# Performance work log

Hardware: AMD Instinct MI355X
Metric: run time of the kernel (lower is better)

Reference implementation:

```python
import jax, jax.numpy as jnp
import numpy as np

N_EVENTS = 4_000_000
HW = 128          # DVS sensor resolution
TICKS = 10_000    # simulation horizon
KH, KW = 3, 3     # kernel_size
OUT_CH = 64       # out_channels


def setup_inputs() -> dict:
    key = jax.random.key(0)
    k1, k2, k3 = jax.random.split(key, 3)
    return {
        "values": jnp.ones((N_EVENTS,), dtype=jnp.float32),            # spike value 1.0 per add_spike
        "ticks_in": jax.random.randint(k1, (N_EVENTS,), 0, TICKS, dtype=jnp.int32),
        "xs": jax.random.randint(k2, (N_EVENTS,), 0, HW, dtype=jnp.int32),
        "ys": jax.random.randint(k3, (N_EVENTS,), 0, HW, dtype=jnp.int32),
        "stride": 1,
    }


def reference(values, ticks_in, xs, ys, stride):
    """Event-driven spike routing of Conv2dT.forward.

    Returns the per-channel synapse input buffers [OUT_CH, KH*KW, TICKS]:
    buffer[c, s, t] = total spike value scattered into synapse s of soma c at tick t.
    (The subsequent izh-soma ODE simulation lives in the external ABM model.)
    """
    S = KH * KW
    off_y = jnp.repeat(jnp.arange(KH), KW)   # [S], ky per synapse_idx = ky*KW + kx
    off_x = jnp.tile(jnp.arange(KW), KH)     # [S], kx per synapse_idx

    out_x = xs[None, :] - off_x[:, None]     # [S, N]
    out_y = ys[None, :] - off_y[:, None]     # [S, N]
    valid = (out_x >= 0) & (out_y >= 0) & (out_x % stride == 0) & (out_y % stride == 0)
    contrib = jnp.where(valid, values[None, :], jnp.zeros((), values.dtype))  # [S, N]

    # scatter-add over ticks for each synapse offset
    buf = jnp.zeros((S, TICKS), dtype=values.dtype)
    buf = buf.at[jnp.arange(S)[:, None], ticks_in[None, :]].add(contrib)     # [S, T]

    # every output channel receives the identical spike dispatch
    return jnp.broadcast_to(buf[None], (OUT_CH, S, TICKS))
```

## Files before the change

### kernel.cpp

```cpp
#include <hip/hip_runtime.h>

#define TICKS 10000
#define NSYN 9
#define OUT_CH 64

#define NPART 32
#define SCATTER_BLOCKS 512
#define SCATTER_THREADS 1024

__global__ void zero_kernel(float* __restrict__ p, int n) {
    int i = blockIdx.x * blockDim.x + threadIdx.x;
    if (i < n) p[i] = 0.0f;
}

__global__ __launch_bounds__(SCATTER_THREADS) void scatter_kernel(
    const float* __restrict__ values,
    const int*   __restrict__ ticks,
    const int*   __restrict__ xs,
    const int*   __restrict__ ys,
    const int*   __restrict__ stride_p,
    float*       __restrict__ buf,
    float*       __restrict__ part,
    int P,
    int n)
{
    __shared__ float lhist[TICKS];
    const int stride = stride_p[0];
    const int tid = threadIdx.x;

    if (stride == 1) {
        for (int j = tid; j < TICKS; j += SCATTER_THREADS) lhist[j] = 0.0f;
        __syncthreads();

        const int n4  = n >> 2;
        const int gsz = gridDim.x * SCATTER_THREADS;
        const float4* __restrict__ v4 = (const float4*)values;
        const int4*   __restrict__ t4 = (const int4*)ticks;
        const int4*   __restrict__ x4 = (const int4*)xs;
        const int4*   __restrict__ y4 = (const int4*)ys;

        for (int i = blockIdx.x * SCATTER_THREADS + tid; i < n4; i += gsz) {
            float4 v = v4[i];
            int4   t = t4[i];
            int4   x = x4[i];
            int4   y = y4[i];

            if (x.x >= 2 && y.x >= 2) atomicAdd(&lhist[t.x], v.x);
            else atomicAdd(&buf[(min(y.x, 2) * 3 + min(x.x, 2)) * TICKS + t.x], v.x);

            if (x.y >= 2 && y.y >= 2) atomicAdd(&lhist[t.y], v.y);
            else atomicAdd(&buf[(min(y.y, 2) * 3 + min(x.y, 2)) * TICKS + t.y], v.y);

            if (x.z >= 2 && y.z >= 2) atomicAdd(&lhist[t.z], v.z);
            else atomicAdd(&buf[(min(y.z, 2) * 3 + min(x.z, 2)) * TICKS + t.z], v.z);

            if (x.w >= 2 && y.w >= 2) atomicAdd(&lhist[t.w], v.w);
            else atomicAdd(&buf[(min(y.w, 2) * 3 + min(x.w, 2)) * TICKS + t.w], v.w);
        }

        if ((n & 3) && blockIdx.x == 0 && tid == 0) {
            for (int i = n4 << 2; i < n; ++i) {
                int cls = min(ys[i], 2) * 3 + min(xs[i], 2);
                if (cls == 8) atomicAdd(&part[ticks[i]], values[i]);
                else          atomicAdd(&buf[cls * TICKS + ticks[i]], values[i]);
            }
        }

        __syncthreads();

        float* __restrict__ dst = part + (size_t)(blockIdx.x % P) * TICKS;
        int phase = ((blockIdx.x / P) * 613) % TICKS;
        for (int j = tid; j < TICKS; j += SCATTER_THREADS) {
            int b = j + phase;
            if (b >= TICKS) b -= TICKS;
            float v = lhist[b];
            if (v != 0.0f) atomicAdd(&dst[b], v);
        }
    } else {
        const int gsz = gridDim.x * SCATTER_THREADS;
        for (int i = blockIdx.x * SCATTER_THREADS + tid; i < n; i += gsz) {
            float v = values[i];
            int   t = ticks[i];
            int   x = xs[i];
            int   y = ys[i];
            #pragma unroll
            for (int ky = 0; ky < 3; ++ky) {
                int oy = y - ky;
                if (oy < 0 || (oy % stride) != 0) continue;
                #pragma unroll
                for (int kx = 0; kx < 3; ++kx) {
                    int ox = x - kx;
                    if (ox < 0 || (ox % stride) != 0) continue;
                    atomicAdd(&buf[(ky * 3 + kx) * TICKS + t], v);
                }
            }
        }
    }
}

__global__ __launch_bounds__(256) void combine_kernel(
    float*       __restrict__ buf,
    const float* __restrict__ part,
    const int*   __restrict__ stride_p,
    int P)
{
    int t = blockIdx.x * blockDim.x + threadIdx.x;
    if (t >= TICKS) return;
    const int stride = stride_p[0];

    float b[NSYN];
    #pragma unroll
    for (int s = 0; s < NSYN; ++s) b[s] = buf[s * TICKS + t];

    if (stride == 1) {
        float s8 = 0.0f;
        for (int p = 0; p < P; ++p) s8 += part[(size_t)p * TICKS + t];
        b[8] = s8;
        #pragma unroll
        for (int r = 0; r < 3; ++r) {
            b[r * 3 + 1] += b[r * 3 + 2];
            b[r * 3 + 0] += b[r * 3 + 1];
        }
        #pragma unroll
        for (int c = 0; c < 3; ++c) {
            b[3 + c] += b[6 + c];
            b[0 + c] += b[3 + c];
        }
    }

    #pragma unroll
    for (int s = 0; s < NSYN; ++s) buf[s * TICKS + t] = b[s];
}

__global__ __launch_bounds__(256) void emit_kernel(
    const float* __restrict__ buf,
    float*       __restrict__ out)
{
    const int T4 = TICKS / 4;
    int t = blockIdx.x * blockDim.x + threadIdx.x;
    if (t >= T4) return;

    const float4* __restrict__ b4 = (const float4*)buf;
    float4*       __restrict__ o4 = (float4*)out;

    float4 b[NSYN];
    #pragma unroll
    for (int s = 0; s < NSYN; ++s) b[s] = b4[s * T4 + t];

    for (int c = blockIdx.y; c < OUT_CH; c += gridDim.y) {
        #pragma unroll
        for (int s = 0; s < NSYN; ++s) {
            o4[(c * NSYN + s) * T4 + t] = b[s];
        }
    }
}

extern "C" void kernel_launch(void* const* d_in, const int* in_sizes, int n_in,
                              void* d_out, int out_size, void* d_ws, size_t ws_size,
                              hipStream_t stream) {
    const float* values   = (const float*)d_in[0];
    const int*   ticks    = (const int*)  d_in[1];
    const int*   xs       = (const int*)  d_in[2];
    const int*   ys       = (const int*)  d_in[3];
    const int*   stride_p = (const int*)  d_in[4];
    float*       out      = (float*)      d_out;
    const int n = in_sizes[0];

    const size_t need = (size_t)(NSYN + NPART) * TICKS * sizeof(float);
    float* buf;
    float* part;
    int    P;
    bool   fallback;
    if (ws_size >= need) {
        buf = (float*)d_ws;
        part = buf + (size_t)NSYN * TICKS;
        P = NPART;
        fallback = false;
    } else {
        buf = out;
        part = buf + (size_t)8 * TICKS;
        P = 1;
        fallback = true;
    }

    {
        int nz = (fallback ? NSYN : (NSYN + NPART)) * TICKS;
        zero_kernel<<<(nz + 255) / 256, 256, 0, stream>>>(buf, nz);
    }

    scatter_kernel<<<SCATTER_BLOCKS, SCATTER_THREADS, 0, stream>>>(
        values, ticks, xs, ys, stride_p, buf, part, P, n);

    combine_kernel<<<(TICKS + 255) / 256, 256, 0, stream>>>(buf, part, stride_p, P);

    {
        dim3 grid((TICKS / 4 + 255) / 256, fallback ? 1 : 64);
        emit_kernel<<<grid, 256, 0, stream>>>(buf, out);
    }
}
```

Baseline: 146.7 us.

## Write per-block tick histograms directly and reduce them in a split combine pass

Each scatter block now stores its full shared-memory histogram to its own partial row with plain float4 stores, replacing atomic adds into a small set of shared partial rows. The scatter grid is halved so there are fewer rows to reduce. A 2D combine kernel sums slices of rows and atomically adds them into synapse 8. The prefix-sum fold over the 3x3 synapse grid moves into the emit kernel. This removes global atomic contention at the end of the scatter, and in exchange it writes and re-reads 256 full histogram rows (about 10 MB) and adds atomics in the combine.

```diff
diff --git a/kernel.cpp b/kernel.cpp
--- a/kernel.cpp
+++ b/kernel.cpp
@@ -4,9 +4,9 @@
 #define NSYN 9
 #define OUT_CH 64
 
-#define NPART 32
-#define SCATTER_BLOCKS 512
+#define SCATTER_BLOCKS 256
 #define SCATTER_THREADS 1024
+#define COMBINE_BY 8
 
 __global__ void zero_kernel(float* __restrict__ p, int n) {
     int i = blockIdx.x * blockDim.x + threadIdx.x;
@@ -61,20 +61,25 @@
         if ((n & 3) && blockIdx.x == 0 && tid == 0) {
             for (int i = n4 << 2; i < n; ++i) {
                 int cls = min(ys[i], 2) * 3 + min(xs[i], 2);
-                if (cls == 8) atomicAdd(&part[ticks[i]], values[i]);
-                else          atomicAdd(&buf[cls * TICKS + ticks[i]], values[i]);
+                atomicAdd(&buf[cls * TICKS + ticks[i]], values[i]);
             }
         }
 
         __syncthreads();
 
-        float* __restrict__ dst = part + (size_t)(blockIdx.x % P) * TICKS;
-        int phase = ((blockIdx.x / P) * 613) % TICKS;
-        for (int j = tid; j < TICKS; j += SCATTER_THREADS) {
-            int b = j + phase;
-            if (b >= TICKS) b -= TICKS;
-            float v = lhist[b];
-            if (v != 0.0f) atomicAdd(&dst[b], v);
+        if (P > 0) {
+            const float4* __restrict__ l4 = (const float4*)lhist;
+            float4* __restrict__ dst = (float4*)(part + (size_t)blockIdx.x * TICKS);
+            const int T4 = TICKS / 4;
+            for (int j = tid; j < T4; j += SCATTER_THREADS) dst[j] = l4[j];
+        } else {
+            int phase = (blockIdx.x * 157) % TICKS;
+            for (int j = tid; j < TICKS; j += SCATTER_THREADS) {
+                int b = j + phase;
+                if (b >= TICKS) b -= TICKS;
+                float v = lhist[b];
+                if (v != 0.0f) atomicAdd(&buf[8 * TICKS + b], v);
+            }
         }
     } else {
         const int gsz = gridDim.x * SCATTER_THREADS;
@@ -104,41 +109,36 @@
     const int*   __restrict__ stride_p,
     int P)
 {
-    int t = blockIdx.x * blockDim.x + threadIdx.x;
-    if (t >= TICKS) return;
-    const int stride = stride_p[0];
-
-    float b[NSYN];
-    #pragma unroll
-    for (int s = 0; s < NSYN; ++s) b[s] = buf[s * TICKS + t];
-
-    if (stride == 1) {
-        float s8 = 0.0f;
-        for (int p = 0; p < P; ++p) s8 += part[(size_t)p * TICKS + t];
-        b[8] = s8;
-        #pragma unroll
-        for (int r = 0; r < 3; ++r) {
-            b[r * 3 + 1] += b[r * 3 + 2];
-            b[r * 3 + 0] += b[r * 3 + 1];
-        }
-        #pragma unroll
-        for (int c = 0; c < 3; ++c) {
-            b[3 + c] += b[6 + c];
-            b[0 + c] += b[3 + c];
-        }
-    }
-
-    #pragma unroll
-    for (int s = 0; s < NSYN; ++s) buf[s * TICKS + t] = b[s];
+    if (stride_p[0] != 1 || P <= 0) return;
+    const int T4 = TICKS / 4;
+    int t4 = blockIdx.x * blockDim.x + threadIdx.x;
+    if (t4 >= T4) return;
+
+    const int rows = P / COMBINE_BY;
+    const int r0   = blockIdx.y * rows;
+    const float4* __restrict__ p4 = (const float4*)part;
+
+    float4 s = make_float4(0.f, 0.f, 0.f, 0.f);
+    for (int r = r0; r < r0 + rows; ++r) {
+        float4 v = p4[(size_t)r * T4 + t4];
+        s.x += v.x; s.y += v.y; s.z += v.z; s.w += v.w;
+    }
+    float* dst = buf + 8 * TICKS + 4 * t4;
+    atomicAdd(dst + 0, s.x);
+    atomicAdd(dst + 1, s.y);
+    atomicAdd(dst + 2, s.z);
+    atomicAdd(dst + 3, s.w);
 }
 
 __global__ __launch_bounds__(256) void emit_kernel(
     const float* __restrict__ buf,
+    const int*   __restrict__ stride_p,
     float*       __restrict__ out)
 {
     const int T4 = TICKS / 4;
     int t = blockIdx.x * blockDim.x + threadIdx.x;
     if (t >= T4) return;
+    const int stride = stride_p[0];
 
     const float4* __restrict__ b4 = (const float4*)buf;
     float4*       __restrict__ o4 = (float4*)out;
@@ -146,6 +146,22 @@
     float4 b[NSYN];
     #pragma unroll
     for (int s = 0; s < NSYN; ++s) b[s] = b4[s * T4 + t];
+
+    if (stride == 1) {
+        #pragma unroll
+        for (int r = 0; r < 3; ++r) {
+            int i2 = r * 3 + 2, i1 = r * 3 + 1, i0 = r * 3;
+            b[i1].x += b[i2].x; b[i1].y += b[i2].y; b[i1].z += b[i2].z; b[i1].w += b[i2].w;
+            b[i0].x += b[i1].x; b[i0].y += b[i1].y; b[i0].z += b[i1].z; b[i0].w += b[i1].w;
+        }
+        #pragma unroll
+        for (int c = 0; c < 3; ++c) {
+            b[3 + c].x += b[6 + c].x; b[3 + c].y += b[6 + c].y;
+            b[3 + c].z += b[6 + c].z; b[3 + c].w += b[6 + c].w;
+            b[0 + c].x += b[3 + c].x; b[0 + c].y += b[3 + c].y;
+            b[0 + c].z += b[3 + c].z; b[0 + c].w += b[3 + c].w;
+        }
+    }
 
     for (int c = blockIdx.y; c < OUT_CH; c += gridDim.y) {
         #pragma unroll
@@ -166,7 +182,7 @@
     float*       out      = (float*)      d_out;
     const int n = in_sizes[0];
 
-    const size_t need = (size_t)(NSYN + NPART) * TICKS * sizeof(float);
+    const size_t need = (size_t)(NSYN + SCATTER_BLOCKS) * TICKS * sizeof(float);
     float* buf;
     float* part;
     int    P;
@@ -174,27 +190,30 @@
     if (ws_size >= need) {
         buf = (float*)d_ws;
         part = buf + (size_t)NSYN * TICKS;
-        P = NPART;
+        P = SCATTER_BLOCKS;
         fallback = false;
     } else {
         buf = out;
-        part = buf + (size_t)8 * TICKS;
-        P = 1;
+        part = buf;
+        P = 0;
         fallback = true;
     }
 
     {
-        int nz = (fallback ? NSYN : (NSYN + NPART)) * TICKS;
+        int nz = NSYN * TICKS;
         zero_kernel<<<(nz + 255) / 256, 256, 0, stream>>>(buf, nz);
     }
 
     scatter_kernel<<<SCATTER_BLOCKS, SCATTER_THREADS, 0, stream>>>(
         values, ticks, xs, ys, stride_p, buf, part, P, n);
 
-    combine_kernel<<<(TICKS + 255) / 256, 256, 0, stream>>>(buf, part, stride_p, P);
+    {
+        dim3 grid((TICKS / 4 + 255) / 256, COMBINE_BY);
+        combine_kernel<<<grid, 256, 0, stream>>>(buf, part, stride_p, P);
+    }
 
     {
         dim3 grid((TICKS / 4 + 255) / 256, fallback ? 1 : 64);
-        emit_kernel<<<grid, 256, 0, stream>>>(buf, out);
-    }
-}
+        emit_kernel<<<grid, 256, 0, stream>>>(buf, stride_p, out);
+    }
+}
```

Result: faster. 135.6 us (-7.6%).
